# Performance work log

Measured on AMD Instinct MI355X. Metric: run time of the kernel, lower is better.

The kernel has to match this reference:

```python
import jax, jax.numpy as jnp
import numpy as np

NTOKENS = 8192   # max_ntokens
TOPK = 2
H = 1024         # hidden
FFN = 4096       # ffn_hidden = 4*hidden
E = 8            # nexperts
M = NTOKENS * TOPK          # total dispatched rows (flux_m_max)
CAP = M // E                # balanced rows per expert


def setup_inputs() -> dict:
    key = jax.random.key(0)
    k1, k2, k3, k4 = jax.random.split(key, 4)
    x = jax.random.normal(k1, (NTOKENS, H), jnp.float32)
    weight0 = jax.random.normal(k2, (E, H, FFN), jnp.float32) * 0.02
    weight1 = jax.random.normal(k3, (E, FFN, H), jnp.float32) * 0.02
    # Balanced routing: scatter_index[t, k] is the row in the expert-sorted
    # dispatched buffer; a permutation of arange(M) gives exactly CAP rows/expert.
    scatter_index = jax.random.permutation(k4, M).reshape(NTOKENS, TOPK).astype(jnp.int32)
    splits = jnp.full((E,), CAP, dtype=jnp.int32)  # rows per expert, sum == M
    return {"x": x, "weight0": weight0, "weight1": weight1,
            "scatter_index": scatter_index, "splits": splits}


def reference(x, weight0, weight1, scatter_index, splits):
    ntokens, topk = scatter_index.shape
    n_exp, h, ffn = weight0.shape
    m = ntokens * topk
    cap = m // n_exp  # splits are balanced by construction (== splits[e])
    # --- AG-scatter: place each (token, k) replica at its dispatched row ---
    vals = jnp.repeat(x, topk, axis=0)                              # [M, h]
    dispatched = jnp.zeros((m, h), x.dtype).at[scatter_index.reshape(-1)].set(vals)
    xe = dispatched.reshape(n_exp, cap, h)                          # [E, C, h]
    # --- grouped GEMM 0 + exact GELU (torch F.gelu default = erf form) ---
    mid = jax.nn.gelu(jnp.einsum('ech,ehf->ecf', xe, weight0), approximate=False)
    # --- grouped GEMM 1 ---
    ye = jnp.einsum('ecf,efh->ech', mid, weight1).reshape(m, h)     # [M, h]
    # --- gather-RS: combine topk expert outputs per token ---
    return ye[scatter_index].sum(axis=1)                            # [ntokens, h]
```

## Files before the change

kernel.cpp:

```cpp
#include <hip/hip_runtime.h>
#include <hip/hip_bf16.h>
#include <cstdint>

constexpr int NT   = 8192;
constexpr int TOPK = 2;
constexpr int H    = 1024;
constexpr int FFN  = 4096;
constexpr int E    = 8;
constexpr int M    = NT * TOPK;
constexpr int CAP  = M / E;

typedef unsigned short u16;
typedef short short8 __attribute__((ext_vector_type(8)));
typedef float f32x4 __attribute__((ext_vector_type(4)));

__device__ __forceinline__ u16 f2bf(float f) {
  union { float f; unsigned u; } c{f};
  unsigned r = (c.u + 0x7FFFu + ((c.u >> 16) & 1u)) >> 16;
  return (u16)r;
}
__device__ __forceinline__ float bf2f(u16 u) {
  union { unsigned u; float f; } c{((unsigned)u) << 16};
  return c.f;
}
__device__ __forceinline__ void async16(const void* g, void* l) {
  auto gp = reinterpret_cast<const __attribute__((address_space(1))) unsigned*>(
      reinterpret_cast<uintptr_t>(g));
  auto lp = reinterpret_cast<__attribute__((address_space(3))) unsigned*>(
      reinterpret_cast<uintptr_t>(l));
  __builtin_amdgcn_global_load_lds(gp, lp, 16, 0, 0);
}

__global__ void scatter_cast_kernel(const float* __restrict__ x,
                                    const int* __restrict__ sidx,
                                    u16* __restrict__ disp) {
  const int t = blockIdx.x;
  const int tid = threadIdx.x;
  const int r0 = sidx[2 * t + 0];
  const int r1 = sidx[2 * t + 1];
  float4 v = ((const float4*)(x + (size_t)t * H))[tid];
  ushort4 b;
  b.x = f2bf(v.x); b.y = f2bf(v.y); b.z = f2bf(v.z); b.w = f2bf(v.w);
  ((ushort4*)disp)[(size_t)r0 * (H / 4) + tid] = b;
  ((ushort4*)disp)[(size_t)r1 * (H / 4) + tid] = b;
}

__global__ __launch_bounds__(256)
void transpose_cvt_kernel(const float* __restrict__ W,
                          u16* __restrict__ WT,
                          int K, int N) {
  __shared__ float tile[64][65];
  const int e = blockIdx.z;
  const float* Wp = W + (size_t)e * K * N;
  u16* Tp = WT + (size_t)e * K * N;
  const int k0 = blockIdx.y * 64;
  const int n0 = blockIdx.x * 64;
  const int tid = threadIdx.x;

  const int u  = tid & 15;
  const int krb = tid >> 4;
#pragma unroll
  for (int p = 0; p < 4; ++p) {
    const int kr = p * 16 + krb;
    float4 v = *(const float4*)&Wp[(size_t)(k0 + kr) * N + n0 + u * 4];
    tile[kr][u * 4 + 0] = v.x;
    tile[kr][u * 4 + 1] = v.y;
    tile[kr][u * 4 + 2] = v.z;
    tile[kr][u * 4 + 3] = v.w;
  }
  __syncthreads();

  const int n  = tid >> 3;
  const int cb = tid & 7;
#pragma unroll
  for (int p = 0; p < 2; ++p) {
    const int nn = p * 32 + n;
    const int c  = cb;
    u16 pack[8];
#pragma unroll
    for (int j = 0; j < 8; ++j) pack[j] = f2bf(tile[c * 8 + j][nn]);
    *(short8*)&Tp[(size_t)(n0 + nn) * K + k0 + c * 8] = *(short8*)pack;
  }
}

template <bool GELU>
__global__ __launch_bounds__(256)
void gemm_bt_kernel(const u16* __restrict__ A,
                    const u16* __restrict__ Bt,
                    u16* __restrict__ C,
                    int Mn, int Nn, int Kn, int nx, int ny) {
  __shared__ __align__(16) u16 lA[128 * 64];
  __shared__ __align__(16) u16 lB[128 * 64];

  const int b = blockIdx.x;
  const int e = b & 7;
  const int t = b >> 3;
  const int q = t & 15, s = t >> 4;
  const int sy = ny >> 2;
  const int sm = s % sy, sn = s / sy;
  const int tm = sm * 4 + (q & 3), tn = sn * 4 + (q >> 2);
  const int m0 = tm * 128, n0 = tn * 128;
  (void)nx;

  const u16* Ae = A  + (size_t)e * Mn * Kn + (size_t)m0 * Kn;
  const u16* Be = Bt + (size_t)e * Nn * Kn + (size_t)n0 * Kn;
  u16* Ce = C + (size_t)e * Mn * Nn;

  const int tid  = threadIdx.x;
  const int lane = tid & 63;
  const int wave = tid >> 6;
  const int wr = wave >> 1, wc = wave & 1;
  const int lhi = lane >> 4, llo = lane & 15;

  const int sr = lane >> 3;
  const int gc = (lane & 7) ^ sr;

  f32x4 acc[4][4] = {};

  for (int kt = 0; kt < Kn; kt += 64) {
#pragma unroll
    for (int s2 = 0; s2 < 4; ++s2) {
      const int i = wave * 4 + s2;
      const int row = i * 8 + sr;
      async16(Ae + (size_t)row * Kn + kt + gc * 8, &lA[i * 512]);
      async16(Be + (size_t)row * Kn + kt + gc * 8, &lB[i * 512]);
    }
    __syncthreads();

#pragma unroll 1
    for (int ks = 0; ks < 2; ++ks) {
      short8 af[4], bf[4];
#pragma unroll
      for (int i = 0; i < 4; ++i) {
        const int row = wr * 64 + i * 16 + llo;
        const int pc = (ks * 4 + lhi) ^ (llo & 7);
        af[i] = *(const short8*)&lA[row * 64 + pc * 8];
      }
#pragma unroll
      for (int j = 0; j < 4; ++j) {
        const int row = wc * 64 + j * 16 + llo;
        const int pc = (ks * 4 + lhi) ^ (llo & 7);
        bf[j] = *(const short8*)&lB[row * 64 + pc * 8];
      }
#pragma unroll
      for (int i = 0; i < 4; ++i)
#pragma unroll
        for (int j = 0; j < 4; ++j)
          acc[i][j] = __builtin_amdgcn_mfma_f32_16x16x32_bf16(af[i], bf[j], acc[i][j], 0, 0, 0);
    }
    __syncthreads();
  }

#pragma unroll
  for (int i = 0; i < 4; ++i) {
    const int mrow = m0 + wr * 64 + i * 16 + lhi * 4;
#pragma unroll
    for (int j = 0; j < 4; ++j) {
      const int ncol = n0 + wc * 64 + j * 16 + llo;
#pragma unroll
      for (int r = 0; r < 4; ++r) {
        float v = acc[i][j][r];
        if (GELU) v = 0.5f * v * (1.0f + erff(v * 0.70710678118654752f));
        Ce[(size_t)(mrow + r) * Nn + ncol] = f2bf(v);
      }
    }
  }
}

__global__ void gather_sum_kernel(const u16* __restrict__ ye,
                                  const int* __restrict__ sidx,
                                  float* __restrict__ out) {
  const int t = blockIdx.x;
  const int tid = threadIdx.x;
  const int r0 = sidx[2 * t + 0];
  const int r1 = sidx[2 * t + 1];
  ushort4 a = ((const ushort4*)ye)[(size_t)r0 * (H / 4) + tid];
  ushort4 b = ((const ushort4*)ye)[(size_t)r1 * (H / 4) + tid];
  float4 s;
  s.x = bf2f(a.x) + bf2f(b.x);
  s.y = bf2f(a.y) + bf2f(b.y);
  s.z = bf2f(a.z) + bf2f(b.z);
  s.w = bf2f(a.w) + bf2f(b.w);
  ((float4*)out)[(size_t)t * (H / 4) + tid] = s;
}

extern "C" void kernel_launch(void* const* d_in, const int* in_sizes, int n_in,
                              void* d_out, int out_size, void* d_ws, size_t ws_size,
                              hipStream_t stream) {
  (void)in_sizes; (void)n_in; (void)out_size; (void)ws_size;
  const float* x    = (const float*)d_in[0];
  const float* w0   = (const float*)d_in[1];
  const float* w1   = (const float*)d_in[2];
  const int*   sidx = (const int*)d_in[3];
  float* out = (float*)d_out;

  char* ws = (char*)d_ws;
  u16* wt   = (u16*)ws;
  u16* disp = (u16*)(ws + (size_t)E * FFN * H * 2);
  u16* mid  = (u16*)(ws + (size_t)E * FFN * H * 2 + (size_t)M * H * 2);
  u16* ye   = disp;

  scatter_cast_kernel<<<NT, 256, 0, stream>>>(x, sidx, disp);
  transpose_cvt_kernel<<<dim3(FFN / 64, H / 64, E), 256, 0, stream>>>(w0, wt, H, FFN);
  gemm_bt_kernel<true><<<dim3((FFN / 128) * (CAP / 128) * E), 256, 0, stream>>>(
      disp, wt, mid, CAP, FFN, H, FFN / 128, CAP / 128);
  transpose_cvt_kernel<<<dim3(H / 64, FFN / 64, E), 256, 0, stream>>>(w1, wt, FFN, H);
  gemm_bt_kernel<false><<<dim3((H / 128) * (CAP / 128) * E), 256, 0, stream>>>(
      mid, wt, ye, CAP, H, FFN, H / 128, CAP / 128);
  gather_sum_kernel<<<NT, 256, 0, stream>>>(ye, sidx, out);
}
```

Measured before the change: 698.8 us.

## Fuse prep kernels, overlap W1 transpose with GEMM0, atomically scatter GEMM1 output

Merges the scatter-cast, the W0 transpose, building the inverse index and zeroing the output into one pre-kernel launch. When the workspace is large enough, the W1 transpose blocks are interleaved into the GEMM0 grid so they run alongside the matmul. GEMM1 now atomically adds its fp32 accumulators straight into each token's output row through the inverse index, which removes the bf16 ye round trip and the gather kernel. Float atomics make the summation order nondeterministic and add atomic traffic, and the ks loop is now fully unrolled.

Result: slower. 730.3 us (+4.5%).

```diff
diff --git a/kernel.cpp b/kernel.cpp
--- a/kernel.cpp
+++ b/kernel.cpp
@@ -3,25 +3,22 @@
 #include <cstdint>
 
 constexpr int NT   = 8192;
-constexpr int TOPK = 2;
 constexpr int H    = 1024;
 constexpr int FFN  = 4096;
 constexpr int E    = 8;
-constexpr int M    = NT * TOPK;
+constexpr int M    = NT * 2;
 constexpr int CAP  = M / E;
 
 typedef unsigned short u16;
 typedef short short8 __attribute__((ext_vector_type(8)));
 typedef float f32x4 __attribute__((ext_vector_type(4)));
+
+__device__ int g_inv[M];
 
 __device__ __forceinline__ u16 f2bf(float f) {
   union { float f; unsigned u; } c{f};
   unsigned r = (c.u + 0x7FFFu + ((c.u >> 16) & 1u)) >> 16;
   return (u16)r;
-}
-__device__ __forceinline__ float bf2f(u16 u) {
-  union { unsigned u; float f; } c{((unsigned)u) << 16};
-  return c.f;
 }
 __device__ __forceinline__ void async16(const void* g, void* l) {
   auto gp = reinterpret_cast<const __attribute__((address_space(1))) unsigned*>(
@@ -31,34 +28,23 @@
   __builtin_amdgcn_global_load_lds(gp, lp, 16, 0, 0);
 }
 
-__global__ void scatter_cast_kernel(const float* __restrict__ x,
-                                    const int* __restrict__ sidx,
-                                    u16* __restrict__ disp) {
-  const int t = blockIdx.x;
-  const int tid = threadIdx.x;
-  const int r0 = sidx[2 * t + 0];
-  const int r1 = sidx[2 * t + 1];
-  float4 v = ((const float4*)(x + (size_t)t * H))[tid];
-  ushort4 b;
-  b.x = f2bf(v.x); b.y = f2bf(v.y); b.z = f2bf(v.z); b.w = f2bf(v.w);
-  ((ushort4*)disp)[(size_t)r0 * (H / 4) + tid] = b;
-  ((ushort4*)disp)[(size_t)r1 * (H / 4) + tid] = b;
-}
-
-__global__ __launch_bounds__(256)
-void transpose_cvt_kernel(const float* __restrict__ W,
-                          u16* __restrict__ WT,
-                          int K, int N) {
-  __shared__ float tile[64][65];
-  const int e = blockIdx.z;
+__device__ __forceinline__ void transpose_body(const float* __restrict__ W,
+                                               u16* __restrict__ WT,
+                                               int K, int N, int tb,
+                                               void* smem_) {
+  float (*tile)[65] = (float(*)[65])smem_;
+  const int ntx = N >> 6;
+  const int per = ntx * (K >> 6);
+  const int e   = tb / per;
+  const int rem = tb - e * per;
+  const int bx  = rem % ntx;
+  const int by  = rem / ntx;
   const float* Wp = W + (size_t)e * K * N;
   u16* Tp = WT + (size_t)e * K * N;
-  const int k0 = blockIdx.y * 64;
-  const int n0 = blockIdx.x * 64;
+  const int k0 = by * 64, n0 = bx * 64;
   const int tid = threadIdx.x;
 
-  const int u  = tid & 15;
-  const int krb = tid >> 4;
+  const int u = tid & 15, krb = tid >> 4;
 #pragma unroll
   for (int p = 0; p < 4; ++p) {
     const int kr = p * 16 + krb;
@@ -70,29 +56,70 @@
   }
   __syncthreads();
 
-  const int n  = tid >> 3;
-  const int cb = tid & 7;
+  const int n = tid >> 3, cb = tid & 7;
 #pragma unroll
   for (int p = 0; p < 2; ++p) {
     const int nn = p * 32 + n;
-    const int c  = cb;
     u16 pack[8];
 #pragma unroll
-    for (int j = 0; j < 8; ++j) pack[j] = f2bf(tile[c * 8 + j][nn]);
-    *(short8*)&Tp[(size_t)(n0 + nn) * K + k0 + c * 8] = *(short8*)pack;
-  }
-}
-
-template <bool GELU>
+    for (int j = 0; j < 8; ++j) pack[j] = f2bf(tile[cb * 8 + j][nn]);
+    *(short8*)&Tp[(size_t)(n0 + nn) * K + k0 + cb * 8] = *(short8*)pack;
+  }
+}
+
+__global__ __launch_bounds__(256)
+void pre_kernel(const float* __restrict__ x, const float* __restrict__ w0,
+                const int* __restrict__ sidx, u16* __restrict__ wt0,
+                u16* __restrict__ disp, float* __restrict__ outz) {
+  __shared__ float tile[64][65];
+  const int b = blockIdx.x;
+  const int tid = threadIdx.x;
+  if (b < 8192) {
+    transpose_body(w0, wt0, H, FFN, b, tile);
+    return;
+  }
+  if (b < 16384) {
+    const int t = b - 8192;
+    const int r0 = sidx[2 * t + 0];
+    const int r1 = sidx[2 * t + 1];
+    float4 v = ((const float4*)(x + (size_t)t * H))[tid];
+    ushort4 bb;
+    bb.x = f2bf(v.x); bb.y = f2bf(v.y); bb.z = f2bf(v.z); bb.w = f2bf(v.w);
+    ((ushort4*)disp)[(size_t)r0 * (H / 4) + tid] = bb;
+    ((ushort4*)disp)[(size_t)r1 * (H / 4) + tid] = bb;
+    return;
+  }
+  if (b < 16448) {
+    const int i = (b - 16384) * 256 + tid;
+    g_inv[sidx[i]] = i >> 1;
+    return;
+  }
+  const int zb = b - 16448;
+  float4 z = {0.f, 0.f, 0.f, 0.f};
+#pragma unroll
+  for (int p = 0; p < 4; ++p)
+    ((float4*)outz)[(size_t)zb * 1024 + p * 256 + tid] = z;
+}
+
+template <bool GELU, bool ATOMIC>
 __global__ __launch_bounds__(256)
 void gemm_bt_kernel(const u16* __restrict__ A,
                     const u16* __restrict__ Bt,
                     u16* __restrict__ C,
-                    int Mn, int Nn, int Kn, int nx, int ny) {
-  __shared__ __align__(16) u16 lA[128 * 64];
-  __shared__ __align__(16) u16 lB[128 * 64];
-
-  const int b = blockIdx.x;
+                    float* __restrict__ outp,
+                    int Mn, int Nn, int Kn, int ny,
+                    const float* __restrict__ Wx, u16* __restrict__ WTx,
+                    int Kx, int Nx) {
+  __shared__ __align__(16) char smem[32768];
+  int b = blockIdx.x;
+  if (Wx != nullptr) {
+    const int g = b / 3, r = b - g * 3;
+    if (r != 0) { transpose_body(Wx, WTx, Kx, Nx, g * 2 + (r - 1), smem); return; }
+    b = g;
+  }
+  u16* lA = (u16*)smem;
+  u16* lB = (u16*)(smem + 16384);
+
   const int e = b & 7;
   const int t = b >> 3;
   const int q = t & 15, s = t >> 4;
@@ -100,11 +127,9 @@
   const int sm = s % sy, sn = s / sy;
   const int tm = sm * 4 + (q & 3), tn = sn * 4 + (q >> 2);
   const int m0 = tm * 128, n0 = tn * 128;
-  (void)nx;
 
   const u16* Ae = A  + (size_t)e * Mn * Kn + (size_t)m0 * Kn;
   const u16* Be = Bt + (size_t)e * Nn * Kn + (size_t)n0 * Kn;
-  u16* Ce = C + (size_t)e * Mn * Nn;
 
   const int tid  = threadIdx.x;
   const int lane = tid & 63;
@@ -127,7 +152,7 @@
     }
     __syncthreads();
 
-#pragma unroll 1
+#pragma unroll
     for (int ks = 0; ks < 2; ++ks) {
       short8 af[4], bf[4];
 #pragma unroll
@@ -151,43 +176,50 @@
     __syncthreads();
   }
 
-#pragma unroll
-  for (int i = 0; i < 4; ++i) {
-    const int mrow = m0 + wr * 64 + i * 16 + lhi * 4;
-#pragma unroll
-    for (int j = 0; j < 4; ++j) {
-      const int ncol = n0 + wc * 64 + j * 16 + llo;
+  if (!ATOMIC) {
+    u16* Ce = C + (size_t)e * Mn * Nn;
+#pragma unroll
+    for (int i = 0; i < 4; ++i) {
+      const int mrow = m0 + wr * 64 + i * 16 + lhi * 4;
+#pragma unroll
+      for (int j = 0; j < 4; ++j) {
+        const int ncol = n0 + wc * 64 + j * 16 + llo;
+#pragma unroll
+        for (int r = 0; r < 4; ++r) {
+          float v = acc[i][j][r];
+          if (GELU) v = 0.5f * v * (1.0f + erff(v * 0.70710678118654752f));
+          Ce[(size_t)(mrow + r) * Nn + ncol] = f2bf(v);
+        }
+      }
+    }
+  } else {
+    const int grBase = e * Mn + m0 + wr * 64;
+#pragma unroll
+    for (int i = 0; i < 4; ++i) {
+      const int rb = grBase + i * 16 + lhi * 4;
 #pragma unroll
       for (int r = 0; r < 4; ++r) {
-        float v = acc[i][j][r];
-        if (GELU) v = 0.5f * v * (1.0f + erff(v * 0.70710678118654752f));
-        Ce[(size_t)(mrow + r) * Nn + ncol] = f2bf(v);
-      }
-    }
-  }
-}
-
-__global__ void gather_sum_kernel(const u16* __restrict__ ye,
-                                  const int* __restrict__ sidx,
-                                  float* __restrict__ out) {
-  const int t = blockIdx.x;
-  const int tid = threadIdx.x;
-  const int r0 = sidx[2 * t + 0];
-  const int r1 = sidx[2 * t + 1];
-  ushort4 a = ((const ushort4*)ye)[(size_t)r0 * (H / 4) + tid];
-  ushort4 b = ((const ushort4*)ye)[(size_t)r1 * (H / 4) + tid];
-  float4 s;
-  s.x = bf2f(a.x) + bf2f(b.x);
-  s.y = bf2f(a.y) + bf2f(b.y);
-  s.z = bf2f(a.z) + bf2f(b.z);
-  s.w = bf2f(a.w) + bf2f(b.w);
-  ((float4*)out)[(size_t)t * (H / 4) + tid] = s;
+        const int tok = g_inv[rb + r];
+        float* orow = outp + (size_t)tok * H + n0 + wc * 64 + llo;
+#pragma unroll
+        for (int j = 0; j < 4; ++j)
+          atomicAdd(orow + j * 16, acc[i][j][r]);
+      }
+    }
+  }
+}
+
+__global__ __launch_bounds__(256)
+void transpose_cvt_kernel(const float* __restrict__ W, u16* __restrict__ WT,
+                          int K, int N) {
+  __shared__ float tile[64][65];
+  transpose_body(W, WT, K, N, blockIdx.x, tile);
 }
 
 extern "C" void kernel_launch(void* const* d_in, const int* in_sizes, int n_in,
                               void* d_out, int out_size, void* d_ws, size_t ws_size,
                               hipStream_t stream) {
-  (void)in_sizes; (void)n_in; (void)out_size; (void)ws_size;
+  (void)in_sizes; (void)n_in; (void)out_size;
   const float* x    = (const float*)d_in[0];
   const float* w0   = (const float*)d_in[1];
   const float* w1   = (const float*)d_in[2];
@@ -195,17 +227,24 @@
   float* out = (float*)d_out;
 
   char* ws = (char*)d_ws;
-  u16* wt   = (u16*)ws;
-  u16* disp = (u16*)(ws + (size_t)E * FFN * H * 2);
-  u16* mid  = (u16*)(ws + (size_t)E * FFN * H * 2 + (size_t)M * H * 2);
-  u16* ye   = disp;
-
-  scatter_cast_kernel<<<NT, 256, 0, stream>>>(x, sidx, disp);
-  transpose_cvt_kernel<<<dim3(FFN / 64, H / 64, E), 256, 0, stream>>>(w0, wt, H, FFN);
-  gemm_bt_kernel<true><<<dim3((FFN / 128) * (CAP / 128) * E), 256, 0, stream>>>(
-      disp, wt, mid, CAP, FFN, H, FFN / 128, CAP / 128);
-  transpose_cvt_kernel<<<dim3(H / 64, FFN / 64, E), 256, 0, stream>>>(w1, wt, FFN, H);
-  gemm_bt_kernel<false><<<dim3((H / 128) * (CAP / 128) * E), 256, 0, stream>>>(
-      mid, wt, ye, CAP, H, FFN, H / 128, CAP / 128);
-  gather_sum_kernel<<<NT, 256, 0, stream>>>(ye, sidx, out);
-}
+  const size_t MB = 1024ull * 1024;
+  u16* wt0  = (u16*)ws;
+  u16* disp = (u16*)(ws + 64 * MB);
+  u16* mid  = (u16*)(ws + 96 * MB);
+  const bool roomy = ws_size >= 288 * MB;
+  u16* wt1 = roomy ? (u16*)(ws + 224 * MB) : wt0;
+
+  pre_kernel<<<18496, 256, 0, stream>>>(x, w0, sidx, wt0, disp, out);
+
+  if (roomy) {
+    gemm_bt_kernel<true, false><<<12288, 256, 0, stream>>>(
+        disp, wt0, mid, nullptr, CAP, FFN, H, CAP / 128, w1, wt1, FFN, H);
+  } else {
+    gemm_bt_kernel<true, false><<<4096, 256, 0, stream>>>(
+        disp, wt0, mid, nullptr, CAP, FFN, H, CAP / 128, nullptr, nullptr, 0, 0);
+    transpose_cvt_kernel<<<8192, 256, 0, stream>>>(w1, wt1, FFN, H);
+  }
+
+  gemm_bt_kernel<false, true><<<1024, 256, 0, stream>>>(
+      mid, wt1, nullptr, out, CAP, H, FFN, CAP / 128, nullptr, nullptr, 0, 0);
+}
```
